# Optimization experiments

Measured on AMD Instinct MI355X. Metric: run time of the kernel, lower is better.

## Reference

```python
import jax, jax.numpy as jnp
import numpy as np

EPS_IN = 1e-5   # InstanceNorm eps
EPS_L1 = 1e-12  # F.normalize eps


def conv1x1(x, w, b):
    # x: [B,C,H,W], w: [O,C], b: [O]
    return jnp.einsum('bchw,oc->bohw', x, w) + b[None, :, None, None]


def conv3x3_reflect(x, w, b):
    xp = jnp.pad(x, ((0, 0), (0, 0), (1, 1), (1, 1)), mode='reflect')
    y = jax.lax.conv_general_dilated(xp, w, (1, 1), 'VALID',
                                     dimension_numbers=('NCHW', 'OIHW', 'NCHW'))
    return y + b[None, :, None, None]


def instance_norm(x):
    mu = x.mean(axis=(2, 3), keepdims=True)
    var = x.var(axis=(2, 3), keepdims=True)  # biased, matches torch InstanceNorm
    return (x - mu) * jax.lax.rsqrt(var + EPS_IN)


def res_block(x, w1, b1, w2, b2):
    h = jax.nn.relu(instance_norm(conv3x3_reflect(x, w1, b1)))
    h = instance_norm(conv3x3_reflect(h, w2, b2))
    return x + h


def _nearest_idx(out_size, in_size):
    # torch F.interpolate(mode='nearest'): src = floor(dst * in/out)
    return (np.arange(out_size) * in_size) // out_size


def forward(x, mask, g_w, g_b, theta_w, theta_b, phi_w, phi_b, W_w, W_b,
            res_w1, res_b1, res_w2, res_b2):
    B, C, H, Wd = x.shape
    N = H * Wd
    g_x = conv1x1(x, g_w, g_b).reshape(B, -1, N).transpose(0, 2, 1)      # [B,N,Ci]
    theta_x = conv1x1(x, theta_w, theta_b).reshape(B, -1, N).transpose(0, 2, 1)
    phi_x = conv1x1(x, phi_w, phi_b).reshape(B, -1, N)                   # [B,Ci,N]
    f = jnp.einsum('bnc,bcm->bnm', theta_x, phi_x)  # temperature = 1.0
    f_div_C = jax.nn.softmax(f, axis=2)
    # mask pipeline
    m = jax.image.resize(mask, (B, 1, H, Wd), method='linear')  # bilinear, half-pixel (align_corners=False)
    m = jnp.where(m > 0, 1.0, m)
    m = 1.0 - m
    hi = _nearest_idx(H, mask.shape[2])
    wi = _nearest_idx(Wd, mask.shape[3])
    tmp = (1.0 - mask)[:, :, hi][:, :, :, wi]  # nearest upsample of (1-mask)
    m = m * tmp                                 # [B,1,H,W]
    f_div_C = f_div_C * m.reshape(B, 1, N)      # broadcast instead of N^2 repeat
    # re_norm=True: L1 renormalize along keys
    f_div_C = f_div_C / jnp.maximum(jnp.sum(jnp.abs(f_div_C), axis=2, keepdims=True), EPS_L1)
    y = jnp.einsum('bnm,bmc->bnc', f_div_C, g_x)             # [B,N,Ci]
    y = y.transpose(0, 2, 1).reshape(B, -1, H, Wd)
    W_y = conv1x1(y, W_w, W_b)
    for i in range(3):
        W_y = res_block(W_y, res_w1[i], res_b1[i], res_w2[i], res_b2[i])
    z = m * x + (1.0 - m) * W_y
    return z


def setup_inputs() -> dict:
    key = jax.random.key(0)
    ks = jax.random.split(key, 16)
    B, C, H, W = 4, 256, 64, 64
    x = jax.random.normal(ks[0], (B, C, H, W), dtype=jnp.float32)
    mask = (jax.random.uniform(ks[1], (B, 1, 32, 32)) < 0.5).astype(jnp.float32)
    s = 0.02
    d = {
        'x': x, 'mask': mask,
        'g_w': jax.random.normal(ks[2], (C, C), jnp.float32) * s,
        'g_b': jnp.zeros((C,), jnp.float32),
        'theta_w': jax.random.normal(ks[3], (C, C), jnp.float32) * s,
        'theta_b': jnp.zeros((C,), jnp.float32),
        'phi_w': jax.random.normal(ks[4], (C, C), jnp.float32) * s,
        'phi_b': jnp.zeros((C,), jnp.float32),
        'W_w': jax.random.normal(ks[5], (C, C), jnp.float32) * s,
        'W_b': jnp.zeros((C,), jnp.float32),
        'res_w1': jax.random.normal(ks[6], (3, C, C, 3, 3), jnp.float32) * s,
        'res_b1': jnp.zeros((3, C), jnp.float32),
        'res_w2': jax.random.normal(ks[7], (3, C, C, 3, 3), jnp.float32) * s,
        'res_b2': jnp.zeros((3, C), jnp.float32),
    }
    return d


def reference(x, mask, g_w, g_b, theta_w, theta_b, phi_w, phi_b, W_w, W_b,
              res_w1, res_b1, res_w2, res_b2):
    return forward(x, mask, g_w, g_b, theta_w, theta_b, phi_w, phi_b, W_w, W_b,
                   res_w1, res_b1, res_w2, res_b2)
```

## Files before the change

### kernel.cpp

```cpp
#include <hip/hip_runtime.h>

#define BB   4
#define CC   256
#define NPIX 4096
#define PB   1048576
#define NTOT 16384

typedef __attribute__((ext_vector_type(8))) short bf16x8;
typedef __attribute__((ext_vector_type(4))) float f32x4;
typedef __attribute__((ext_vector_type(4))) unsigned short u16x4;

__device__ __forceinline__ unsigned short f2b(float f) {
  union { float f; unsigned u; } v; v.f = f;
  unsigned r = v.u + 0x7fffu + ((v.u >> 16) & 1u);
  return (unsigned short)(r >> 16);
}
__device__ __forceinline__ float b2f(unsigned short h) {
  union { unsigned u; float f; } v; v.u = ((unsigned)h) << 16;
  return v.f;
}
__device__ __forceinline__ f32x4 mfma16(bf16x8 a, bf16x8 b, f32x4 c) {
  return __builtin_amdgcn_mfma_f32_16x16x32_bf16(a, b, c, 0, 0, 0);
}
__device__ __forceinline__ void gload_lds16(const unsigned short* g, unsigned short* l) {
  __builtin_amdgcn_global_load_lds(
      (const __attribute__((address_space(1))) unsigned int*)g,
      (__attribute__((address_space(3))) unsigned int*)l, 16, 0, 0);
}
__device__ __forceinline__ int remap_px(int n, int dh, int dw) {
  int h = (n >> 6) + dh;
  int w = (n & 63) + dw;
  h = h < 0 ? 1 : (h > 63 ? 62 : h);
  w = w < 0 ? 1 : (w > 63 ? 62 : w);
  return (h << 6) | w;
}

__global__ void repack_w1x1_k(const float* __restrict__ tw, const float* __restrict__ pw,
                              const float* __restrict__ gw, const float* __restrict__ Ww,
                              unsigned short* __restrict__ dst) {
  int i = blockIdx.x * 256 + threadIdx.x;
  dst[i]           = f2b(tw[i]);
  dst[65536 + i]   = f2b(pw[i]);
  dst[131072 + i]  = f2b(gw[i]);
  dst[196608 + i]  = f2b(Ww[i]);
}

__global__ void repack_bias_k(const float* __restrict__ tb, const float* __restrict__ pb,
                              const float* __restrict__ gb, const float* __restrict__ Wb,
                              float* __restrict__ bias) {
  int i = blockIdx.x * 256 + threadIdx.x;
  float v;
  if (i < 256) v = tb[i];
  else if (i < 512) v = pb[i - 256];
  else if (i < 768) v = gb[i - 512];
  else v = Wb[i - 768];
  bias[i] = v;
}

__global__ void repack_res_k(const float* __restrict__ w1, const float* __restrict__ w2,
                             unsigned short* __restrict__ wk) {
  int idx = blockIdx.x * 256 + threadIdx.x;
  if (idx >= 1769472) return;
  int t = idx % 9;
  int rest = idx / 9;
  int c = rest & 255;
  int o = (rest >> 8) & 255;
  int i = rest >> 16;
  size_t d = (size_t)t * 65536 + o * 256 + c;
  wk[(size_t)(2 * i)     * 589824 + d] = f2b(w1[idx]);
  wk[(size_t)(2 * i + 1) * 589824 + d] = f2b(w2[idx]);
}

__global__ void prep_mask_k(const float* __restrict__ mask, float* __restrict__ m) {
  int idx = blockIdx.x * 256 + threadIdx.x;
  if (idx >= BB * NPIX) return;
  int b = idx >> 12, n = idx & 4095;
  int h = n >> 6, w = n & 63;
  const float* M = mask + b * 1024;
  float sh = 0.5f * h - 0.25f, sw = 0.5f * w - 0.25f;
  int h0 = (int)floorf(sh), w0 = (int)floorf(sw);
  float th = sh - h0, tw = sw - w0;
  int h0c = min(max(h0, 0), 31), h1c = min(max(h0 + 1, 0), 31);
  int w0c = min(max(w0, 0), 31), w1c = min(max(w0 + 1, 0), 31);
  float v = (1.f - th) * ((1.f - tw) * M[h0c * 32 + w0c] + tw * M[h0c * 32 + w1c])
          +        th  * ((1.f - tw) * M[h1c * 32 + w0c] + tw * M[h1c * 32 + w1c]);
  float inv = v > 0.f ? 0.f : 1.f;
  float tmp = 1.f - M[(h >> 1) * 32 + (w >> 1)];
  m[idx] = inv * tmp;
}

__global__ void mask_scan_k(const float* __restrict__ mbuf, int* __restrict__ ci,
                            int* __restrict__ kcount) {
  int b = blockIdx.x;
  int tid = threadIdx.x;
  __shared__ int sc[256];
  const float* mb = mbuf + b * 4096;
  int n0 = tid * 16, cnt = 0;
  float mv[16];
  #pragma unroll
  for (int i = 0; i < 16; ++i) { mv[i] = mb[n0 + i]; cnt += mv[i] > 0.f ? 1 : 0; }
  sc[tid] = cnt;
  __syncthreads();
  for (int off = 1; off < 256; off <<= 1) {
    int v = sc[tid];
    int u = tid >= off ? sc[tid - off] : 0;
    __syncthreads();
    sc[tid] = v + u;
    __syncthreads();
  }
  int base = sc[tid] - cnt;
  int* cib = ci + b * 4096;
  #pragma unroll
  for (int i = 0; i < 16; ++i)
    if (mv[i] > 0.f) cib[base++] = n0 + i;
  if (tid == 255) kcount[b] = sc[255];
}

__global__ void gather_phi_k(const unsigned short* __restrict__ phb, const int* __restrict__ ci,
                             const int* __restrict__ kcount, unsigned short* __restrict__ phic) {
  int b = blockIdx.y;
  int Kb = kcount[b];
  int pad = (Kb + 63) & ~63;
  int j = blockIdx.x * 8 + (threadIdx.x >> 5);
  int cl = threadIdx.x & 31;
  if (j >= pad) return;
  bf16x8 v;
  if (j < Kb) {
    v = *(const bf16x8*)(phb + (size_t)b * PB + (size_t)ci[b * 4096 + j] * 256 + cl * 8);
  } else {
    for (int t = 0; t < 8; ++t) v[t] = 0;
  }
  *(bf16x8*)(phic + (size_t)b * PB + (size_t)j * 256 + cl * 8) = v;
}

__global__ void gather_g_k(const unsigned short* __restrict__ gbuf, const int* __restrict__ ci,
                           const int* __restrict__ kcount, unsigned short* __restrict__ gc) {
  int b = blockIdx.z;
  int Kb = kcount[b];
  int pad = (Kb + 63) & ~63;
  int c = blockIdx.y;
  int j = blockIdx.x * 256 + threadIdx.x;
  if (j >= pad) return;
  unsigned short v = 0;
  if (j < Kb) v = gbuf[(size_t)c * NTOT + b * 4096 + ci[b * 4096 + j]];
  gc[(size_t)c * NTOT + b * 4096 + j] = v;
}

__global__ void transpose_x_k(const float* __restrict__ x, unsigned short* __restrict__ xT) {
  __shared__ float T[64][65];
  int b = blockIdx.z;
  int n0 = blockIdx.x * 64, c0 = blockIdx.y * 64;
  int tx = threadIdx.x, ty = threadIdx.y;
  const float* xb = x + (size_t)b * PB;
  #pragma unroll
  for (int i = 0; i < 16; ++i) {
    int cl = ty + i * 4;
    T[cl][tx] = xb[(size_t)(c0 + cl) * NPIX + n0 + tx];
  }
  __syncthreads();
  unsigned short* ob = xT + (size_t)b * PB;
  #pragma unroll
  for (int i = 0; i < 16; ++i) {
    int nl = ty + i * 4;
    ob[(size_t)(n0 + nl) * CC + c0 + tx] = f2b(T[tx][nl]);
  }
}

template <int EPI, int TAPS, int KSPLIT>
__launch_bounds__(256, 2)
__global__ void gemm_w(const unsigned short* __restrict__ A,
                       const unsigned short* __restrict__ Bact,
                       const float* __restrict__ bias,
                       float* __restrict__ outF,
                       unsigned short* __restrict__ o0,
                       unsigned short* __restrict__ o1,
                       unsigned short* __restrict__ o2) {
  int m0 = blockIdx.y * 128;
  int bxs = (blockIdx.x & 7) * 16 + (blockIdx.x >> 3);
  int n0 = bxs * 128;
  int tid = threadIdx.x, lane = tid & 63, wid = tid >> 6;
  int wm = wid >> 1, wn = wid & 1;
  int r16 = lane & 15, g4 = lane >> 4;
  __shared__ __align__(16) unsigned short As[2 * 8192];
  __shared__ __align__(16) unsigned short Bs[2 * 8192];
  f32x4 acc[4][4] = {};
  int r0 = tid >> 3;
  int scol = ((((tid * 16) & 127) ^ ((r0 & 7) << 4)) >> 1);
  int q7 = r16 & 7;
  int ra[4], rbv[4];
  #pragma unroll
  for (int i = 0; i < 4; ++i) ra[i] = (wm * 64 + i * 16 + r16) * 128;
  #pragma unroll
  for (int j = 0; j < 4; ++j) rbv[j] = (wn * 64 + j * 16 + r16) * 128;

  const int nsteps = TAPS * 4;
  const int span = nsteps / KSPLIT;
  const int s0 = (KSPLIT > 1 ? blockIdx.z : 0) * span;
  const int s1 = s0 + span;

#define STAGE(st_, bs_) do {                                                      \
    int tap_ = (st_) >> 2, k0_ = ((st_) & 3) * 64;                                \
    const unsigned short* At_ = A + tap_ * 65536;                                 \
    _Pragma("unroll")                                                             \
    for (int q = 0; q < 4; ++q)                                                   \
      gload_lds16(At_ + (size_t)(m0 + r0 + q * 32) * 256 + k0_ + scol,            \
                  &As[(bs_) * 8192 + tid * 8 + q * 2048]);                        \
    _Pragma("unroll")                                                             \
    for (int q = 0; q < 4; ++q) {                                                 \
      int n_ = n0 + r0 + q * 32;                                                  \
      int bsrc_ = n_;                                                             \
      if (TAPS == 9) bsrc_ = (n_ & ~4095) | remap_px(n_ & 4095, tap_ / 3 - 1, tap_ % 3 - 1); \
      gload_lds16(Bact + (size_t)bsrc_ * 256 + k0_ + scol,                        \
                  &Bs[(bs_) * 8192 + tid * 8 + q * 2048]);                        \
    }                                                                             \
  } while (0)

#define COMPUTE(bs_) do {                                                         \
    _Pragma("unroll")                                                             \
    for (int kk = 0; kk < 2; ++kk) {                                              \
      bf16x8 af_[4], bf_[4];                                                      \
      _Pragma("unroll")                                                           \
      for (int i = 0; i < 4; ++i)                                                 \
        af_[i] = *(const bf16x8*)((const char*)As + (bs_) * 16384 + ra[i] +       \
                                  (((kk * 4 + g4) ^ q7) << 4));                   \
      _Pragma("unroll")                                                           \
      for (int j = 0; j < 4; ++j)                                                 \
        bf_[j] = *(const bf16x8*)((const char*)Bs + (bs_) * 16384 + rbv[j] +      \
                                  (((kk * 4 + g4) ^ q7) << 4));                   \
      _Pragma("unroll")                                                           \
      for (int i = 0; i < 4; ++i)                                                 \
        _Pragma("unroll")                                                         \
        for (int j = 0; j < 4; ++j)                                               \
          acc[i][j] = mfma16(af_[i], bf_[j], acc[i][j]);                          \
    }                                                                             \
  } while (0)

  STAGE(s0, 0);
  for (int st = s0; st < s1; ++st) {
    __syncthreads();
    if (st + 1 < s1) STAGE(st + 1, (st + 1 - s0) & 1);
    COMPUTE((st - s0) & 1);
  }
#undef STAGE
#undef COMPUTE

  #pragma unroll
  for (int i = 0; i < 4; ++i) {
    int row = m0 + wm * 64 + i * 16 + g4 * 4;
    #pragma unroll
    for (int j = 0; j < 4; ++j) {
      int n = n0 + wn * 64 + j * 16 + r16;
      f32x4 v = acc[i][j];
      if constexpr (EPI == 0) {
        int sec = row >> 8;
        int ch = row & 255;
        if (sec < 2) {
          u16x4 pk;
          #pragma unroll
          for (int r = 0; r < 4; ++r) pk[r] = f2b(v[r] + bias[row + r]);
          *(u16x4*)((sec ? o1 : o0) + (size_t)n * 256 + ch) = pk;
        } else {
          #pragma unroll
          for (int r = 0; r < 4; ++r)
            o2[(size_t)(ch + r) * NTOT + n] = f2b(v[r] + bias[row + r]);
        }
      } else if constexpr (EPI == 1) {
        u16x4 pk;
        #pragma unroll
        for (int r = 0; r < 4; ++r) pk[r] = f2b(v[r]);
        *(u16x4*)(o0 + (size_t)n * 256 + row) = pk;
      } else if constexpr (EPI == 2) {
        #pragma unroll
        for (int r = 0; r < 4; ++r) v[r] += bias[row + r];
        *(f32x4*)(outF + (size_t)n * 256 + row) = v;
        u16x4 pk;
        #pragma unroll
        for (int r = 0; r < 4; ++r) pk[r] = f2b(v[r]);
        *(u16x4*)(o0 + (size_t)n * 256 + row) = pk;
      } else {
        float* dst = blockIdx.z ? (float*)o0 : outF;
        *(f32x4*)&dst[(size_t)n * 256 + row] = v;
      }
    }
  }
}

__global__ void combine_stats_k(const float* __restrict__ p0, const float* __restrict__ p1,
                                unsigned short* __restrict__ cb,
                                float* __restrict__ psum, float* __restrict__ psq) {
  int p = blockIdx.x;
  int b = blockIdx.y;
  int tid = threadIdx.x;
  int cg = (tid & 31) * 8;
  int rsub = tid >> 5;
  size_t base = ((size_t)b * 4096 + p * 128) * 256;
  float s[8] = {}, s2[8] = {};
  for (int it = 0; it < 16; ++it) {
    int row = rsub + it * 8;
    size_t e = base + (size_t)row * 256 + cg;
    f32x4 a0 = *(const f32x4*)&p0[e];
    f32x4 a1 = *(const f32x4*)&p0[e + 4];
    f32x4 c0 = *(const f32x4*)&p1[e];
    f32x4 c1 = *(const f32x4*)&p1[e + 4];
    bf16x8 ov;
    #pragma unroll
    for (int j = 0; j < 4; ++j) {
      float f = a0[j] + c0[j];
      ov[j] = (short)f2b(f); s[j] += f; s2[j] += f * f;
    }
    #pragma unroll
    for (int j = 0; j < 4; ++j) {
      float f = a1[j] + c1[j];
      ov[4 + j] = (short)f2b(f); s[4 + j] += f; s2[4 + j] += f * f;
    }
    *(bf16x8*)&cb[e] = ov;
  }
  __shared__ float redS[8][256];
  __shared__ float redQ[8][256];
  #pragma unroll
  for (int j = 0; j < 8; ++j) { redS[rsub][cg + j] = s[j]; redQ[rsub][cg + j] = s2[j]; }
  __syncthreads();
  float a = 0.f, q = 0.f;
  #pragma unroll
  for (int r = 0; r < 8; ++r) { a += redS[r][tid]; q += redQ[r][tid]; }
  int o = (p * BB + b) * CC + tid;
  psum[o] = a; psq[o] = q;
}

__launch_bounds__(512, 2)
__global__ void attn_k(const unsigned short* __restrict__ theta,
                       const unsigned short* __restrict__ phic,
                       const unsigned short* __restrict__ gc,
                       const int* __restrict__ kcount,
                       float* __restrict__ Op0,
                       float* __restrict__ Op1,
                       float2* __restrict__ ml2) {
  int f = blockIdx.x;
  int b = (f & 7) >> 1;
  int s = f & 1;
  int q0 = (f >> 3) * 128;
  int tid = threadIdx.x, lane = tid & 63, wid = tid >> 6;
  int r16 = lane & 15, g4 = lane >> 4;
  const unsigned short* th = theta + (size_t)b * PB;
  const unsigned short* phb = phic + (size_t)b * PB;

  int Kb = kcount[b];
  int nt = (Kb + 63) >> 6;
  int h = (nt + 1) >> 1;
  int t0 = s * h, t1 = min(nt, t0 + h);

  __shared__ __align__(16) unsigned short Kt[2][16384];
  __shared__ __align__(16) unsigned short Vt[2][16384];
  __shared__ __align__(16) unsigned short Plds[8][16][72];

  int qrow = q0 + wid * 16 + r16;
  bf16x8 aq[8];
  #pragma unroll
  for (int ks = 0; ks < 8; ++ks)
    aq[ks] = *(const bf16x8*)(th + (size_t)qrow * CC + ks * 32 + 8 * g4);

  f32x4 O[16];
  #pragma unroll
  for (int cf = 0; cf < 16; ++cf) { O[cf][0] = 0.f; O[cf][1] = 0.f; O[cf][2] = 0.f; O[cf][3] = 0.f; }
  float mrow[4] = {-1e30f, -1e30f, -1e30f, -1e30f};
  float lrow[4] = {0.f, 0.f, 0.f, 0.f};

  bf16x8 kst[4], vst[4];
  if (t0 < t1) {
    int k0g = t0 * 64;
    #pragma unroll
    for (int i = 0; i < 4; ++i) {
      int slot = wid * 4 + i;
      kst[i] = *(const bf16x8*)(phb + (size_t)(k0g + lane) * CC + slot * 8);
      vst[i] = *(const bf16x8*)(gc + (size_t)(i * 64 + lane) * NTOT + b * 4096 + k0g + wid * 8);
    }
    #pragma unroll
    for (int i = 0; i < 4; ++i) {
      int slot = wid * 4 + i;
      *(bf16x8*)&Kt[0][slot * 512 + lane * 8] = kst[i];
      *(bf16x8*)&Vt[0][wid * 2048 + i * 512 + lane * 8] = vst[i];
    }
  }
  __syncthreads();

  #pragma unroll 1
  for (int t = t0; t < t1; ++t) {
    int p = (t - t0) & 1;
    if (t + 1 < t1) {
      int k0g = (t + 1) * 64;
      #pragma unroll
      for (int i = 0; i < 4; ++i) {
        int slot = wid * 4 + i;
        kst[i] = *(const bf16x8*)(phb + (size_t)(k0g + lane) * CC + slot * 8);
        vst[i] = *(const bf16x8*)(gc + (size_t)(i * 64 + lane) * NTOT + b * 4096 + k0g + wid * 8);
      }
    }
    f32x4 S[4];
    #pragma unroll
    for (int ff = 0; ff < 4; ++ff) { S[ff][0] = 0.f; S[ff][1] = 0.f; S[ff][2] = 0.f; S[ff][3] = 0.f; }
    #pragma unroll
    for (int ks = 0; ks < 8; ++ks) {
      #pragma unroll
      for (int ff = 0; ff < 4; ++ff) {
        bf16x8 bk = *(const bf16x8*)&Kt[p][(ks * 4 + g4) * 512 + (ff * 16 + r16) * 8];
        S[ff] = mfma16(aq[ks], bk, S[ff]);
      }
    }
    bool mk[4];
    #pragma unroll
    for (int ff = 0; ff < 4; ++ff) mk[ff] = (t * 64 + ff * 16 + r16) < Kb;
    float scr[4];
    #pragma unroll
    for (int r = 0; r < 4; ++r) {
      float v = -1e30f;
      #pragma unroll
      for (int ff = 0; ff < 4; ++ff) v = fmaxf(v, mk[ff] ? S[ff][r] : -1e30f);
      v = fmaxf(v, __shfl_xor(v, 1));
      v = fmaxf(v, __shfl_xor(v, 2));
      v = fmaxf(v, __shfl_xor(v, 4));
      v = fmaxf(v, __shfl_xor(v, 8));
      float nm = fmaxf(mrow[r], v);
      scr[r] = __expf(mrow[r] - nm);
      mrow[r] = nm;
      lrow[r] *= scr[r];
    }
    float ps[4][4];
    float rsum[4] = {0.f, 0.f, 0.f, 0.f};
    #pragma unroll
    for (int ff = 0; ff < 4; ++ff)
      #pragma unroll
      for (int r = 0; r < 4; ++r) {
        float pp = mk[ff] ? __expf(S[ff][r] - mrow[r]) : 0.f;
        ps[ff][r] = pp;
        rsum[r] += pp;
      }
    #pragma unroll
    for (int r = 0; r < 4; ++r) {
      float sm = rsum[r];
      sm += __shfl_xor(sm, 1);
      sm += __shfl_xor(sm, 2);
      sm += __shfl_xor(sm, 4);
      sm += __shfl_xor(sm, 8);
      lrow[r] += sm;
    }
    #pragma unroll
    for (int cf = 0; cf < 16; ++cf) {
      O[cf][0] *= scr[0]; O[cf][1] *= scr[1]; O[cf][2] *= scr[2]; O[cf][3] *= scr[3];
    }
    #pragma unroll
    for (int ff = 0; ff < 4; ++ff)
      #pragma unroll
      for (int r = 0; r < 4; ++r)
        Plds[wid][g4 * 4 + r][ff * 16 + r16] = f2b(ps[ff][r]);
    #pragma unroll
    for (int ks2 = 0; ks2 < 2; ++ks2) {
      bf16x8 ap = *(const bf16x8*)&Plds[wid][r16][ks2 * 32 + 8 * g4];
      #pragma unroll
      for (int cf = 0; cf < 16; ++cf) {
        bf16x8 bv = *(const bf16x8*)&Vt[p][(ks2 * 4 + g4) * 2048 + (cf * 16 + r16) * 8];
        O[cf] = mfma16(ap, bv, O[cf]);
      }
    }
    if (t + 1 < t1) {
      #pragma unroll
      for (int i = 0; i < 4; ++i) {
        int slot = wid * 4 + i;
        *(bf16x8*)&Kt[p ^ 1][slot * 512 + lane * 8] = kst[i];
        *(bf16x8*)&Vt[p ^ 1][wid * 2048 + i * 512 + lane * 8] = vst[i];
      }
    }
    __syncthreads();
  }

  float* Opb = (s ? Op1 : Op0) + (size_t)b * NPIX * CC;
  #pragma unroll
  for (int cf = 0; cf < 16; ++cf)
    #pragma unroll
    for (int r = 0; r < 4; ++r)
      Opb[(size_t)(q0 + wid * 16 + g4 * 4 + r) * CC + cf * 16 + r16] = O[cf][r];
  if (r16 == 0) {
    #pragma unroll
    for (int r = 0; r < 4; ++r)
      ml2[(size_t)(s * BB + b) * NPIX + q0 + wid * 16 + g4 * 4 + r] =
          make_float2(mrow[r], lrow[r]);
  }
}

__global__ void attn_combine_k(const float* __restrict__ Op0, const float* __restrict__ Op1,
                               const float2* __restrict__ ml2, unsigned short* __restrict__ y) {
  size_t e = ((size_t)blockIdx.x * 256 + threadIdx.x) * 8;
  int bn = (int)(e >> 8);
  float2 a = ml2[bn];
  float2 c = ml2[16384 + bn];
  float M = fmaxf(a.x, c.x);
  float e0 = __expf(a.x - M), e1 = __expf(c.x - M);
  float L = a.y * e0 + c.y * e1;
  float sc = L > 1e-30f ? 1.f / L : 0.f;
  e0 *= sc; e1 *= sc;
  f32x4 p0 = *(const f32x4*)&Op0[e];
  f32x4 p1 = *(const f32x4*)&Op0[e + 4];
  f32x4 q0 = *(const f32x4*)&Op1[e];
  f32x4 q1 = *(const f32x4*)&Op1[e + 4];
  bf16x8 r;
  #pragma unroll
  for (int j = 0; j < 4; ++j) {
    r[j]     = (short)f2b(p0[j] * e0 + q0[j] * e1);
    r[4 + j] = (short)f2b(p1[j] * e0 + q1[j] * e1);
  }
  *(bf16x8*)&y[e] = r;
}

__global__ void in_finalize_k(const float* __restrict__ psum, const float* __restrict__ psumsq,
                              float* __restrict__ mu, float* __restrict__ rs) {
  int bc = blockIdx.x * 256 + threadIdx.x;
  int b = bc >> 8, c = bc & 255;
  float s = 0.f, s2 = 0.f;
  for (int p = 0; p < 32; ++p) {
    s  += psum[(p * BB + b) * CC + c];
    s2 += psumsq[(p * BB + b) * CC + c];
  }
  float m_ = s * (1.f / 4096.f);
  float var = s2 * (1.f / 4096.f) - m_ * m_;
  var = var > 0.f ? var : 0.f;
  mu[bc] = m_;
  rs[bc] = rsqrtf(var + 1e-5f);
}

__global__ void normrelu_k(const unsigned short* __restrict__ src,
                           const float* __restrict__ mu, const float* __restrict__ rs,
                           unsigned short* __restrict__ dst) {
  size_t idx = (size_t)blockIdx.x * 256 + threadIdx.x;
  size_t e = idx * 8;
  if (e >= (size_t)BB * PB) return;
  int c = (int)(e & 255);
  int b = (int)(e >> 20);
  const float* mup = mu + b * 256 + c;
  const float* rsp = rs + b * 256 + c;
  bf16x8 v = *(const bf16x8*)(src + e);
  bf16x8 ov;
  #pragma unroll
  for (int j = 0; j < 8; ++j) {
    float f = (b2f((unsigned short)v[j]) - mup[j]) * rsp[j];
    ov[j] = (short)f2b(f > 0.f ? f : 0.f);
  }
  *(bf16x8*)(dst + e) = ov;
}

__global__ void resupdate_k(const unsigned short* __restrict__ c2,
                            const float* __restrict__ mu, const float* __restrict__ rs,
                            float* __restrict__ r, unsigned short* __restrict__ rb) {
  size_t idx = (size_t)blockIdx.x * 256 + threadIdx.x;
  size_t e = idx * 8;
  if (e >= (size_t)BB * PB) return;
  int c = (int)(e & 255);
  int b = (int)(e >> 20);
  const float* mup = mu + b * 256 + c;
  const float* rsp = rs + b * 256 + c;
  bf16x8 v = *(const bf16x8*)(c2 + e);
  bf16x8 ov;
  #pragma unroll
  for (int j = 0; j < 8; ++j) {
    float f = r[e + j] + (b2f((unsigned short)v[j]) - mup[j]) * rsp[j];
    r[e + j] = f;
    ov[j] = (short)f2b(f);
  }
  *(bf16x8*)(rb + e) = ov;
}

__global__ void final_blend_k(const float* __restrict__ x, const float* __restrict__ r,
                              const float* __restrict__ m, float* __restrict__ out) {
  __shared__ float T[64][65];
  int b = blockIdx.z;
  int n0 = blockIdx.x * 64, c0 = blockIdx.y * 64;
  int tx = threadIdx.x, ty = threadIdx.y;
  #pragma unroll
  for (int i = 0; i < 16; ++i) {
    int nl = ty + i * 4;
    T[nl][tx] = r[(size_t)b * PB + (size_t)(n0 + nl) * CC + c0 + tx];
  }
  __syncthreads();
  #pragma unroll
  for (int i = 0; i < 16; ++i) {
    int cl = ty + i * 4;
    int cg = c0 + cl, ng = n0 + tx;
    float mv = m[b * NPIX + ng];
    float xv = x[(size_t)b * PB + (size_t)cg * NPIX + ng];
    out[(size_t)b * PB + (size_t)cg * NPIX + ng] = mv * xv + (1.f - mv) * T[tx][cl];
  }
}

#define OFF_M    0UL
#define OFF_XT   65536UL
#define OFF_TH   8454144UL
#define OFF_PH   16842752UL
#define OFF_G    25231360UL
#define OFF_R    33619968UL
#define OFF_W1   50397184UL
#define OFF_WK   50921472UL
#define OFF_MU   57999360UL
#define OFF_RS   58003456UL
#define OFF_PS   58007552UL
#define OFF_PS2  58138624UL
#define OFF_OP1  58269696UL
#define OFF_ML   75046912UL
#define OFF_CI   75309056UL
#define OFF_KC   75374592UL
#define OFF_BIAS 75374848UL

extern "C" void kernel_launch(void* const* d_in, const int* in_sizes, int n_in,
                              void* d_out, int out_size, void* d_ws, size_t ws_size,
                              hipStream_t stream) {
  const float* x       = (const float*)d_in[0];
  const float* maskp   = (const float*)d_in[1];
  const float* g_w     = (const float*)d_in[2];
  const float* g_b     = (const float*)d_in[3];
  const float* theta_w = (const float*)d_in[4];
  const float* theta_b = (const float*)d_in[5];
  const float* phi_w   = (const float*)d_in[6];
  const float* phi_b   = (const float*)d_in[7];
  const float* W_w     = (const float*)d_in[8];
  const float* W_b     = (const float*)d_in[9];
  const float* res_w1  = (const float*)d_in[10];
  const float* res_w2  = (const float*)d_in[12];
  float* out = (float*)d_out;
  char* ws = (char*)d_ws;

  float*          mbuf = (float*)(ws + OFF_M);
  unsigned short* xT   = (unsigned short*)(ws + OFF_XT);
  unsigned short* phic = (unsigned short*)(ws + OFF_XT);
  unsigned short* ybuf = (unsigned short*)(ws + OFF_XT);
  unsigned short* thb  = (unsigned short*)(ws + OFF_TH);
  unsigned short* cbuf = (unsigned short*)(ws + OFF_TH);
  unsigned short* phb  = (unsigned short*)(ws + OFF_PH);
  unsigned short* gc   = (unsigned short*)(ws + OFF_PH);
  unsigned short* hbuf = (unsigned short*)(ws + OFF_PH);
  unsigned short* gbuf = (unsigned short*)(ws + OFF_G);
  unsigned short* rb   = (unsigned short*)(ws + OFF_G);
  float*          rbuf = (float*)(ws + OFF_R);
  float*          aop0 = (float*)(ws + OFF_R);
  float*          aop1 = (float*)(ws + OFF_OP1);
  float*          cp0  = (float*)(ws + OFF_OP1);
  float*          cp1  = out;
  float2*         ml2  = (float2*)(ws + OFF_ML);
  int*            ci   = (int*)(ws + OFF_CI);
  int*            kc   = (int*)(ws + OFF_KC);
  float*          biasS= (float*)(ws + OFF_BIAS);
  unsigned short* thw  = (unsigned short*)(ws + OFF_W1);
  unsigned short* Www  = (unsigned short*)(ws + OFF_W1 + 393216);
  unsigned short* wkres= (unsigned short*)(ws + OFF_WK);
  float*          mu   = (float*)(ws + OFF_MU);
  float*          rs   = (float*)(ws + OFF_RS);
  float*          psum = (float*)(ws + OFF_PS);
  float*          psq  = (float*)(ws + OFF_PS2);

  repack_w1x1_k<<<256, 256, 0, stream>>>(theta_w, phi_w, g_w, W_w, thw);
  repack_res_k<<<6912, 256, 0, stream>>>(res_w1, res_w2, wkres);
  repack_bias_k<<<4, 256, 0, stream>>>(theta_b, phi_b, g_b, W_b, biasS);
  prep_mask_k<<<64, 256, 0, stream>>>(maskp, mbuf);
  transpose_x_k<<<dim3(64, 4, 4), dim3(64, 4), 0, stream>>>(x, xT);

  gemm_w<0, 1, 1><<<dim3(128, 6), 256, 0, stream>>>(thw, xT, biasS, nullptr, thb, phb, gbuf);

  mask_scan_k<<<4, 256, 0, stream>>>(mbuf, ci, kc);
  gather_phi_k<<<dim3(512, 4), 256, 0, stream>>>(phb, ci, kc, phic);
  gather_g_k<<<dim3(16, 256, 4), 256, 0, stream>>>(gbuf, ci, kc, gc);

  attn_k<<<256, 512, 0, stream>>>(thb, phic, gc, kc, aop0, aop1, ml2);
  attn_combine_k<<<2048, 256, 0, stream>>>(aop0, aop1, ml2, ybuf);

  gemm_w<2, 1, 1><<<dim3(128, 2), 256, 0, stream>>>(Www, ybuf, biasS + 768, rbuf, rb,
                                                    nullptr, nullptr);

  for (int i = 0; i < 3; ++i) {
    gemm_w<3, 9, 2><<<dim3(128, 2, 2), 256, 0, stream>>>(
        wkres + (size_t)(2 * i) * 589824, rb, nullptr, cp0,
        (unsigned short*)cp1, nullptr, nullptr);
    combine_stats_k<<<dim3(32, 4), 256, 0, stream>>>(cp0, cp1, cbuf, psum, psq);
    in_finalize_k<<<4, 256, 0, stream>>>(psum, psq, mu, rs);
    normrelu_k<<<2048, 256, 0, stream>>>(cbuf, mu, rs, hbuf);
    gemm_w<3, 9, 2><<<dim3(128, 2, 2), 256, 0, stream>>>(
        wkres + (size_t)(2 * i + 1) * 589824, hbuf, nullptr, cp0,
        (unsigned short*)cp1, nullptr, nullptr);
    combine_stats_k<<<dim3(32, 4), 256, 0, stream>>>(cp0, cp1, cbuf, psum, psq);
    in_finalize_k<<<4, 256, 0, stream>>>(psum, psq, mu, rs);
    resupdate_k<<<2048, 256, 0, stream>>>(cbuf, mu, rs, rbuf, rb);
  }

  final_blend_k<<<dim3(64, 4, 4), dim3(64, 4), 0, stream>>>(x, rbuf, mbuf, out);
}
```

Before: 499.8 us.

## Halve GEMM N-tile to 64 and store split-K conv partials as bf16

The shared GEMM kernel now uses a 128x64 tile instead of 128x128, with half the B staging, half the accumulators and an occupancy hint of three blocks per SM. Grids are doubled so every GEMM launch gets twice as many blocks to fill the machine. Separately, the split-K 3x3 conv partials are written as bf16 instead of fp32, and the stats-combine kernel reads bf16, which halves that intermediate traffic. The cost is less reuse of the A operand per tile and extra rounding of the partial sums before they are added and normalised.

```diff
diff --git a/kernel.cpp b/kernel.cpp
--- a/kernel.cpp
+++ b/kernel.cpp
@@ -167,7 +167,7 @@
 }
 
 template <int EPI, int TAPS, int KSPLIT>
-__launch_bounds__(256, 2)
+__launch_bounds__(256, 3)
 __global__ void gemm_w(const unsigned short* __restrict__ A,
                        const unsigned short* __restrict__ Bact,
                        const float* __restrict__ bias,
@@ -176,22 +176,22 @@
                        unsigned short* __restrict__ o1,
                        unsigned short* __restrict__ o2) {
   int m0 = blockIdx.y * 128;
-  int bxs = (blockIdx.x & 7) * 16 + (blockIdx.x >> 3);
-  int n0 = bxs * 128;
+  int bxs = (blockIdx.x & 7) * 32 + (blockIdx.x >> 3);
+  int n0 = bxs * 64;
   int tid = threadIdx.x, lane = tid & 63, wid = tid >> 6;
   int wm = wid >> 1, wn = wid & 1;
   int r16 = lane & 15, g4 = lane >> 4;
   __shared__ __align__(16) unsigned short As[2 * 8192];
-  __shared__ __align__(16) unsigned short Bs[2 * 8192];
-  f32x4 acc[4][4] = {};
+  __shared__ __align__(16) unsigned short Bs[2 * 4096];
+  f32x4 acc[4][2] = {};
   int r0 = tid >> 3;
   int scol = ((((tid * 16) & 127) ^ ((r0 & 7) << 4)) >> 1);
   int q7 = r16 & 7;
-  int ra[4], rbv[4];
+  int ra[4], rbv[2];
   #pragma unroll
   for (int i = 0; i < 4; ++i) ra[i] = (wm * 64 + i * 16 + r16) * 128;
   #pragma unroll
-  for (int j = 0; j < 4; ++j) rbv[j] = (wn * 64 + j * 16 + r16) * 128;
+  for (int j = 0; j < 2; ++j) rbv[j] = (wn * 32 + j * 16 + r16) * 128;
 
   const int nsteps = TAPS * 4;
   const int span = nsteps / KSPLIT;
@@ -206,31 +206,31 @@
       gload_lds16(At_ + (size_t)(m0 + r0 + q * 32) * 256 + k0_ + scol,            \
                   &As[(bs_) * 8192 + tid * 8 + q * 2048]);                        \
     _Pragma("unroll")                                                             \
-    for (int q = 0; q < 4; ++q) {                                                 \
+    for (int q = 0; q < 2; ++q) {                                                 \
       int n_ = n0 + r0 + q * 32;                                                  \
       int bsrc_ = n_;                                                             \
       if (TAPS == 9) bsrc_ = (n_ & ~4095) | remap_px(n_ & 4095, tap_ / 3 - 1, tap_ % 3 - 1); \
       gload_lds16(Bact + (size_t)bsrc_ * 256 + k0_ + scol,                        \
-                  &Bs[(bs_) * 8192 + tid * 8 + q * 2048]);                        \
+                  &Bs[(bs_) * 4096 + tid * 8 + q * 2048]);                        \
     }                                                                             \
   } while (0)
 
 #define COMPUTE(bs_) do {                                                         \
     _Pragma("unroll")                                                             \
     for (int kk = 0; kk < 2; ++kk) {                                              \
-      bf16x8 af_[4], bf_[4];                                                      \
+      bf16x8 af_[4], bf_[2];                                                      \
       _Pragma("unroll")                                                           \
       for (int i = 0; i < 4; ++i)                                                 \
         af_[i] = *(const bf16x8*)((const char*)As + (bs_) * 16384 + ra[i] +       \
                                   (((kk * 4 + g4) ^ q7) << 4));                   \
       _Pragma("unroll")                                                           \
-      for (int j = 0; j < 4; ++j)                                                 \
-        bf_[j] = *(const bf16x8*)((const char*)Bs + (bs_) * 16384 + rbv[j] +      \
+      for (int j = 0; j < 2; ++j)                                                 \
+        bf_[j] = *(const bf16x8*)((const char*)Bs + (bs_) * 8192 + rbv[j] +       \
                                   (((kk * 4 + g4) ^ q7) << 4));                   \
       _Pragma("unroll")                                                           \
       for (int i = 0; i < 4; ++i)                                                 \
         _Pragma("unroll")                                                         \
-        for (int j = 0; j < 4; ++j)                                               \
+        for (int j = 0; j < 2; ++j)                                               \
           acc[i][j] = mfma16(af_[i], bf_[j], acc[i][j]);                          \
     }                                                                             \
   } while (0)
@@ -248,8 +248,8 @@
   for (int i = 0; i < 4; ++i) {
     int row = m0 + wm * 64 + i * 16 + g4 * 4;
     #pragma unroll
-    for (int j = 0; j < 4; ++j) {
-      int n = n0 + wn * 64 + j * 16 + r16;
+    for (int j = 0; j < 2; ++j) {
+      int n = n0 + wn * 32 + j * 16 + r16;
       f32x4 v = acc[i][j];
       if constexpr (EPI == 0) {
         int sec = row >> 8;
@@ -278,14 +278,18 @@
         for (int r = 0; r < 4; ++r) pk[r] = f2b(v[r]);
         *(u16x4*)(o0 + (size_t)n * 256 + row) = pk;
       } else {
-        float* dst = blockIdx.z ? (float*)o0 : outF;
-        *(f32x4*)&dst[(size_t)n * 256 + row] = v;
+        unsigned short* dst = blockIdx.z ? o1 : o0;
+        u16x4 pk;
+        #pragma unroll
+        for (int r = 0; r < 4; ++r) pk[r] = f2b(v[r]);
+        *(u16x4*)(dst + (size_t)n * 256 + row) = pk;
       }
     }
   }
 }
 
-__global__ void combine_stats_k(const float* __restrict__ p0, const float* __restrict__ p1,
+__global__ void combine_stats_k(const unsigned short* __restrict__ p0,
+                                const unsigned short* __restrict__ p1,
                                 unsigned short* __restrict__ cb,
                                 float* __restrict__ psum, float* __restrict__ psq) {
   int p = blockIdx.x;
@@ -298,20 +302,13 @@
   for (int it = 0; it < 16; ++it) {
     int row = rsub + it * 8;
     size_t e = base + (size_t)row * 256 + cg;
-    f32x4 a0 = *(const f32x4*)&p0[e];
-    f32x4 a1 = *(const f32x4*)&p0[e + 4];
-    f32x4 c0 = *(const f32x4*)&p1[e];
-    f32x4 c1 = *(const f32x4*)&p1[e + 4];
+    bf16x8 a = *(const bf16x8*)&p0[e];
+    bf16x8 c = *(const bf16x8*)&p1[e];
     bf16x8 ov;
     #pragma unroll
-    for (int j = 0; j < 4; ++j) {
-      float f = a0[j] + c0[j];
+    for (int j = 0; j < 8; ++j) {
+      float f = b2f((unsigned short)a[j]) + b2f((unsigned short)c[j]);
       ov[j] = (short)f2b(f); s[j] += f; s2[j] += f * f;
-    }
-    #pragma unroll
-    for (int j = 0; j < 4; ++j) {
-      float f = a1[j] + c1[j];
-      ov[4 + j] = (short)f2b(f); s[4 + j] += f; s2[4 + j] += f * f;
     }
     *(bf16x8*)&cb[e] = ov;
   }
@@ -639,8 +636,8 @@
   float*          rbuf = (float*)(ws + OFF_R);
   float*          aop0 = (float*)(ws + OFF_R);
   float*          aop1 = (float*)(ws + OFF_OP1);
-  float*          cp0  = (float*)(ws + OFF_OP1);
-  float*          cp1  = out;
+  unsigned short* cp0  = (unsigned short*)(ws + OFF_OP1);
+  unsigned short* cp1  = (unsigned short*)out;
   float2*         ml2  = (float2*)(ws + OFF_ML);
   int*            ci   = (int*)(ws + OFF_CI);
   int*            kc   = (int*)(ws + OFF_KC);
@@ -659,7 +656,7 @@
   prep_mask_k<<<64, 256, 0, stream>>>(maskp, mbuf);
   transpose_x_k<<<dim3(64, 4, 4), dim3(64, 4), 0, stream>>>(x, xT);
 
-  gemm_w<0, 1, 1><<<dim3(128, 6), 256, 0, stream>>>(thw, xT, biasS, nullptr, thb, phb, gbuf);
+  gemm_w<0, 1, 1><<<dim3(256, 6), 256, 0, stream>>>(thw, xT, biasS, nullptr, thb, phb, gbuf);
 
   mask_scan_k<<<4, 256, 0, stream>>>(mbuf, ci, kc);
   gather_phi_k<<<dim3(512, 4), 256, 0, stream>>>(phb, ci, kc, phic);
@@ -668,19 +665,17 @@
   attn_k<<<256, 512, 0, stream>>>(thb, phic, gc, kc, aop0, aop1, ml2);
   attn_combine_k<<<2048, 256, 0, stream>>>(aop0, aop1, ml2, ybuf);
 
-  gemm_w<2, 1, 1><<<dim3(128, 2), 256, 0, stream>>>(Www, ybuf, biasS + 768, rbuf, rb,
+  gemm_w<2, 1, 1><<<dim3(256, 2), 256, 0, stream>>>(Www, ybuf, biasS + 768, rbuf, rb,
                                                     nullptr, nullptr);
 
   for (int i = 0; i < 3; ++i) {
-    gemm_w<3, 9, 2><<<dim3(128, 2, 2), 256, 0, stream>>>(
-        wkres + (size_t)(2 * i) * 589824, rb, nullptr, cp0,
-        (unsigned short*)cp1, nullptr, nullptr);
+    gemm_w<3, 9, 2><<<dim3(256, 2, 2), 256, 0, stream>>>(
+        wkres + (size_t)(2 * i) * 589824, rb, nullptr, nullptr, cp0, cp1, nullptr);
     combine_stats_k<<<dim3(32, 4), 256, 0, stream>>>(cp0, cp1, cbuf, psum, psq);
     in_finalize_k<<<4, 256, 0, stream>>>(psum, psq, mu, rs);
     normrelu_k<<<2048, 256, 0, stream>>>(cbuf, mu, rs, hbuf);
-    gemm_w<3, 9, 2><<<dim3(128, 2, 2), 256, 0, stream>>>(
-        wkres + (size_t)(2 * i + 1) * 589824, hbuf, nullptr, cp0,
-        (unsigned short*)cp1, nullptr, nullptr);
+    gemm_w<3, 9, 2><<<dim3(256, 2, 2), 256, 0, stream>>>(
+        wkres + (size_t)(2 * i + 1) * 589824, hbuf, nullptr, nullptr, cp0, cp1, nullptr);
     combine_stats_k<<<dim3(32, 4), 256, 0, stream>>>(cp0, cp1, cbuf, psum, psq);
     in_finalize_k<<<4, 256, 0, stream>>>(psum, psq, mu, rs);
     resupdate_k<<<2048, 256, 0, stream>>>(cbuf, mu, rs, rbuf, rb);
```

Result: slower. 546.0 us (+9.2%).
